# Optimization experiments

Measured on AMD Instinct MI355X. Metric: run time of the kernel, lower is better.

Reference implementation:

```python
import jax, jax.numpy as jnp
import numpy as np

E = 16           # num_experts
D = 4096         # hidden_size
F = 688          # per-expert SwiGLU intermediate size
N = 8192         # total tokens (bsz*seq_len)
CAP_FACTOR = 1.25


def setup_inputs() -> dict:
    key = jax.random.key(0)
    k1, k2, k3, k4, k5, k6 = jax.random.split(key, 6)
    return {
        "x": jax.random.normal(k1, (N, D), dtype=jnp.float32),
        "topk_idx": jax.random.randint(k2, (N,), 0, E, dtype=jnp.int32),
        "topk_scores": jax.random.uniform(k3, (N,), dtype=jnp.float32),
        "Wg": jax.random.normal(k4, (E, D, F), dtype=jnp.float32) * 0.02,
        "Wu": jax.random.normal(k5, (E, D, F), dtype=jnp.float32) * 0.02,
        "Wd": jax.random.normal(k6, (E, F, D), dtype=jnp.float32) * 0.02,
    }


def reference(x, topk_idx, topk_scores, Wg, Wu, Wd):
    # Switch-style top-1 MoE with capacity-based token dropping.
    # Deterministic variant: tokens beyond capacity are dropped in token order
    # (original uses randperm; the math pattern is identical).
    n, d = x.shape
    e = Wg.shape[0]
    cap = int(CAP_FACTOR * n / e)  # static under jit

    # position of each token within its assigned expert (0-based)
    oh = jax.nn.one_hot(topk_idx, e, dtype=jnp.int32)            # [N, E]
    pos = jnp.take_along_axis(jnp.cumsum(oh, axis=0) - 1,
                              topk_idx[:, None].astype(jnp.int32), axis=1)[:, 0]
    keep = pos < cap                                             # [N] bool

    # dispatch: scatter kept tokens into [E, cap, D]; dropped go to dummy row E
    e_safe = jnp.where(keep, topk_idx, e)
    p_safe = jnp.minimum(pos, cap - 1)
    buf = jnp.zeros((e + 1, cap, d), x.dtype).at[e_safe, p_safe].set(x)[:e]

    # per-expert SwiGLU FFN: down(silu(gate(x)) * up(x))
    h = jax.nn.silu(jnp.einsum('ecd,edf->ecf', buf, Wg)) \
        * jnp.einsum('ecd,edf->ecf', buf, Wu)                    # [E, cap, F]
    out = jnp.einsum('ecf,efd->ecd', h, Wd)                      # [E, cap, D]

    # combine: gather back, zero-pad dropped tokens, scale by gate scores
    y = out[topk_idx, p_safe] * keep[:, None].astype(x.dtype)
    y = y * topk_scores[:, None]
    return y
```

## Files before the change

### kernel.cpp

```cpp
#include <hip/hip_runtime.h>
#include <hip/hip_bf16.h>

#define E_ 16
#define D_ 4096
#define F_ 688
#define N_ 8192
#define CAP_ 640
#define NFT_ 11
#define NKT32_ 128
#define NFT32_ 22

typedef __attribute__((ext_vector_type(8))) short bf16x8;
typedef __attribute__((ext_vector_type(4))) float f32x4;
typedef __attribute__((ext_vector_type(4))) float fvec4;
typedef __attribute__((ext_vector_type(4))) unsigned short usvec4;
typedef __attribute__((ext_vector_type(8))) unsigned short usvec8;

__device__ __forceinline__ unsigned short f2bf(float f) {
    __hip_bfloat16 h = __float2bfloat16(f);
    return __builtin_bit_cast(unsigned short, h);
}
__device__ __forceinline__ void gload16(const unsigned short* g, unsigned short* l) {
    __builtin_amdgcn_global_load_lds(
        (const __attribute__((address_space(1))) unsigned int*)g,
        (__attribute__((address_space(3))) unsigned int*)l, 16, 0, 0);
}

#define WAITVN(N) asm volatile("s_waitcnt vmcnt(" #N ")" ::: "memory")
#define SBAR      __builtin_amdgcn_s_barrier()
#define SCHED0    __builtin_amdgcn_sched_barrier(0)


__global__ void k_dispatch(const int* __restrict__ idx,
                           int* __restrict__ slot_token,
                           int* __restrict__ row_of,
                           int* __restrict__ cnt) {
    __shared__ int hist[256][E_];
    const int t = threadIdx.x;
#pragma unroll
    for (int e = 0; e < E_; e++) hist[t][e] = 0;
    __syncthreads();
    const int base = t * (N_ / 256);
    for (int j = 0; j < N_ / 256; j++) {
        int e = idx[base + j];
        hist[t][e]++;
    }
    __syncthreads();
    if (t < E_) {
        int run = 0;
        for (int i = 0; i < 256; i++) { int v = hist[i][t]; hist[i][t] = run; run += v; }
        cnt[t] = run < CAP_ ? run : CAP_;
    }
    for (int s = t; s < E_ * CAP_; s += 256) slot_token[s] = -1;
    __syncthreads();
    for (int j = 0; j < N_ / 256; j++) {
        int i = base + j;
        int e = idx[i];
        int p = hist[t][e]++;
        if (p < CAP_) { slot_token[e * CAP_ + p] = i; row_of[i] = e * CAP_ + p; }
        else          { row_of[i] = -1; }
    }
}

__global__ void k_zero_dropped(const int* __restrict__ row_of, float* __restrict__ y) {
    for (int i = blockIdx.x; i < N_; i += gridDim.x) {
        if (row_of[i] >= 0) continue;
        fvec4* yp = (fvec4*)(y + (size_t)i * D_);
        fvec4 z = {0.f, 0.f, 0.f, 0.f};
        for (int c = threadIdx.x; c < D_ / 4; c += 256) yp[c] = z;
    }
}

__global__ void k_gather(const float* __restrict__ x, const int* __restrict__ slot_token,
                         unsigned short* __restrict__ Aimg) {
    const int strip = blockIdx.y;
    const int kg = blockIdx.x;
    const int t = threadIdx.x;
    const int r = t >> 1, h = t & 1;
    const int tok = slot_token[strip * 128 + r];
#pragma unroll
    for (int i = 0; i < 8; i++) {
        const int kt = kg * 8 + i;
        unsigned short* dst = Aimg + ((size_t)strip * NKT32_ + kt) * 4096;
        usvec8 p0, p1;
        if (tok < 0) {
            usvec8 z = {0, 0, 0, 0, 0, 0, 0, 0};
            p0 = z; p1 = z;
        } else {
            const float* src = x + (size_t)tok * D_ + kt * 32 + h * 16;
            fvec4 a = *(const fvec4*)(src);
            fvec4 b = *(const fvec4*)(src + 4);
            fvec4 c = *(const fvec4*)(src + 8);
            fvec4 d = *(const fvec4*)(src + 12);
            usvec8 q0 = {f2bf(a[0]), f2bf(a[1]), f2bf(a[2]), f2bf(a[3]),
                         f2bf(b[0]), f2bf(b[1]), f2bf(b[2]), f2bf(b[3])};
            usvec8 q1 = {f2bf(c[0]), f2bf(c[1]), f2bf(c[2]), f2bf(c[3]),
                         f2bf(d[0]), f2bf(d[1]), f2bf(d[2]), f2bf(d[3])};
            p0 = q0; p1 = q1;
        }
        *(usvec8*)&dst[(2 * h) * 1024 + r * 8]     = p0;
        *(usvec8*)&dst[(2 * h + 1) * 1024 + r * 8] = p1;
    }
}

__global__ void k_wprep_gu(const float* __restrict__ Wg, const float* __restrict__ Wu,
                           unsigned short* __restrict__ img) {
    const int ft = blockIdx.x, kt = blockIdx.y, e = blockIdx.z;
    const int tid = threadIdx.x;
    const int f4 = (tid & 15) * 4, kq4 = (tid >> 4) * 4;
    const int gf = ft * 64 + f4;
    const bool v = gf < F_;
    const fvec4 fz = {0.f, 0.f, 0.f, 0.f};
    fvec4 g[4], u[4];
#pragma unroll
    for (int r = 0; r < 4; r++) {
        size_t off = (size_t)e * D_ * F_ + (size_t)(kt * 64 + kq4 + r) * F_ + gf;
        g[r] = v ? *(const fvec4*)(Wg + off) : fz;
        u[r] = v ? *(const fvec4*)(Wu + off) : fz;
    }
    const int t32 = kq4 >> 5, kl = kq4 & 31;
    unsigned short* dst = img + ((size_t)(e * NKT32_ + kt * 2 + t32) * NFT_ + ft) * 4096;
    const int ubase = (kl >> 3) * 512 + (kl & 7);
#pragma unroll
    for (int i = 0; i < 4; i++) {
        usvec4 pg = {f2bf(g[0][i]), f2bf(g[1][i]), f2bf(g[2][i]), f2bf(g[3][i])};
        usvec4 pu = {f2bf(u[0][i]), f2bf(u[1][i]), f2bf(u[2][i]), f2bf(u[3][i])};
        *(usvec4*)&dst[ubase + (f4 + i) * 8]        = pg;
        *(usvec4*)&dst[2048 + ubase + (f4 + i) * 8] = pu;
    }
}

__global__ void k_wprep_d(const float* __restrict__ Wd, unsigned short* __restrict__ img) {
    const int dt = blockIdx.x, kt = blockIdx.y, e = blockIdx.z;
    const int tid = threadIdx.x;
    const int d4 = (tid & 15) * 4, kq4 = (tid >> 4) * 4;
    const int gd = dt * 64 + d4;
    const fvec4 fz = {0.f, 0.f, 0.f, 0.f};
    fvec4 b[4];
#pragma unroll
    for (int r = 0; r < 4; r++) {
        int krow = kt * 64 + kq4 + r;
        b[r] = (krow < F_) ? *(const fvec4*)(Wd + (size_t)e * F_ * D_ + (size_t)krow * D_ + gd) : fz;
    }
    const int t32 = kq4 >> 5, kl = kq4 & 31;
    unsigned short* dst = img + ((size_t)(e * NFT32_ + kt * 2 + t32) * 64 + dt) * 2048;
    const int ubase = (kl >> 3) * 512 + (kl & 7);
#pragma unroll
    for (int i = 0; i < 4; i++) {
        usvec4 p = {f2bf(b[0][i]), f2bf(b[1][i]), f2bf(b[2][i]), f2bf(b[3][i])};
        *(usvec4*)&dst[ubase + (d4 + i) * 8] = p;
    }
}

__global__ __launch_bounds__(256, 2) void k_gemm1_dma(
    const unsigned short* __restrict__ Aimg, const unsigned short* __restrict__ Wgu,
    const int* __restrict__ cnt, unsigned short* __restrict__ Himg) {
    const int bid = blockIdx.x;
    const int xcd = bid & 7;
    const int j = bid >> 3;
    const int mb = j % 5;
    const int gl = j / 5;
    const int group = xcd * 22 + gl;
    const int e = group / NFT_, fidx = group % NFT_;
    const int m0 = mb * 128;
    if (m0 >= cnt[e]) return;
    const int strip = e * 5 + mb;

    __shared__ __align__(16) unsigned short Bgu[3][8192];

    const int tid = threadIdx.x;
    const int lane = tid & 63, wave = tid >> 6;
    const int wm = wave & 1, kh = wave >> 1;

    f32x4 accG[4][4], accU[4][4];
#pragma unroll
    for (int a = 0; a < 4; a++)
#pragma unroll
        for (int b = 0; b < 4; b++) {
            f32x4 z = {0.f, 0.f, 0.f, 0.f};
            accG[a][b] = z; accU[a][b] = z;
        }

    const unsigned short* Astrip = Aimg + (size_t)strip * NKT32_ * 4096;
    const unsigned short* WguE = Wgu + ((size_t)e * NKT32_ * NFT_ + fidx) * 4096;
    const int GUS = NFT_ * 4096;
    const int afo = (lane >> 4) * 1024 + (wm * 64 + (lane & 15)) * 8;
    const int bfo = (lane >> 4) * 512 + (lane & 15) * 8;

    bf16x8 a0[4], a1[4];

#define LOADA1(T, S)                                                             \
    {                                                                            \
        const unsigned short* ab = Astrip + (size_t)(2 * (T) + kh) * 4096 + afo; \
        _Pragma("unroll") for (int mf = 0; mf < 4; mf++)                         \
            S[mf] = *(const bf16x8*)(ab + mf * 128);                             \
    }
#define DMAB1(T, BUF)                                                            \
    {                                                                            \
        const unsigned short* bA = WguE + (size_t)(2 * (T)) * GUS;               \
        const unsigned short* bB = bA + GUS;                                     \
        _Pragma("unroll") for (int i = 0; i < 4; i++) {                          \
            const int c = wave * 4 + i;                                          \
            const unsigned short* src = (c < 8) ? (bA + c * 512) : (bB + (c - 8) * 512); \
            gload16(src + lane * 8, &Bgu[BUF][c * 512]);                         \
        }                                                                        \
    }
#define MFMAS1(BUF, S)                                                           \
    {                                                                            \
        __builtin_amdgcn_s_setprio(1);                                           \
        bf16x8 bg[4], bu[4];                                                     \
        _Pragma("unroll") for (int nf = 0; nf < 4; nf++) {                       \
            bg[nf] = *(const bf16x8*)&Bgu[BUF][kh * 4096 + bfo + nf * 128];      \
            bu[nf] = *(const bf16x8*)&Bgu[BUF][kh * 4096 + 2048 + bfo + nf * 128]; \
        }                                                                        \
        _Pragma("unroll") for (int mf = 0; mf < 4; mf++)                         \
        _Pragma("unroll") for (int nf = 0; nf < 4; nf++) {                       \
            accG[mf][nf] = __builtin_amdgcn_mfma_f32_16x16x32_bf16(S[mf], bg[nf], accG[mf][nf], 0, 0, 0); \
            accU[mf][nf] = __builtin_amdgcn_mfma_f32_16x16x32_bf16(S[mf], bu[nf], accU[mf][nf], 0, 0, 0); \
        }                                                                        \
        __builtin_amdgcn_s_setprio(0);                                           \
    }
#define G1IT(T, CS, NS, WN, HA, HB)                                              \
    {                                                                            \
        WAITVN(WN);                                                              \
        SBAR;                                                                    \
        if (HA) { LOADA1((T) + 1, NS) }                                          \
        if (HB) { DMAB1((T) + 2, ((T) + 2) % 3) }                                \
        SCHED0;                                                                  \
        MFMAS1((T) % 3, CS)                                                      \
    }

    LOADA1(0, a0)
    SCHED0;
    DMAB1(0, 0)
    DMAB1(1, 1)
    SCHED0;

    for (int m = 0; m < 31; m++) {
        G1IT(2 * m,     a0, a1, 4, 1, 1)
        G1IT(2 * m + 1, a1, a0, 4, 1, 1)
    }
    G1IT(62, a0, a1, 4, 1, 0)
    G1IT(63, a1, a0, 0, 0, 0)
#undef G1IT
#undef MFMAS1
#undef DMAB1
#undef LOADA1

    {
        float* red = (float*)(&Bgu[0][0]);
#define RED1(ACC)                                                                \
    {                                                                            \
        __syncthreads();                                                         \
        if (kh == 0) {                                                           \
            _Pragma("unroll") for (int mf = 0; mf < 4; mf++)                     \
            _Pragma("unroll") for (int nfl = 0; nfl < 2; nfl++)                  \
                *(f32x4*)&red[(((wm * 2 + 1) * 4 + mf) * 2 + nfl) * 256 + lane * 4] = ACC[mf][2 + nfl]; \
        } else {                                                                 \
            _Pragma("unroll") for (int mf = 0; mf < 4; mf++)                     \
            _Pragma("unroll") for (int nfl = 0; nfl < 2; nfl++)                  \
                *(f32x4*)&red[(((wm * 2 + 0) * 4 + mf) * 2 + nfl) * 256 + lane * 4] = ACC[mf][0 + nfl]; \
        }                                                                        \
        __syncthreads();                                                         \
        if (kh == 0) {                                                           \
            _Pragma("unroll") for (int mf = 0; mf < 4; mf++)                     \
            _Pragma("unroll") for (int nfl = 0; nfl < 2; nfl++) {                \
                f32x4 p = *(const f32x4*)&red[(((wm * 2 + 0) * 4 + mf) * 2 + nfl) * 256 + lane * 4]; \
                ACC[mf][0 + nfl] += p;                                           \
            }                                                                    \
        } else {                                                                 \
            _Pragma("unroll") for (int mf = 0; mf < 4; mf++)                     \
            _Pragma("unroll") for (int nfl = 0; nfl < 2; nfl++) {                \
                f32x4 p = *(const f32x4*)&red[(((wm * 2 + 1) * 4 + mf) * 2 + nfl) * 256 + lane * 4]; \
                ACC[mf][2 + nfl] += p;                                           \
            }                                                                    \
        }                                                                        \
    }
        RED1(accG)
        RED1(accU)
#undef RED1
    }

    unsigned short* Hs = Himg + (size_t)(strip * NFT32_ + fidx * 2) * 4096;
#define EPI1(NB)                                                                 \
    _Pragma("unroll") for (int mf = 0; mf < 4; mf++)                             \
    _Pragma("unroll") for (int nfl = 0; nfl < 2; nfl++) {                        \
        int fl = (NB + nfl) * 16 + (lane & 15);                                  \
        int rl = wm * 64 + mf * 16 + ((lane >> 4) << 2);                         \
        unsigned short* Ht = Hs + (size_t)(fl >> 5) * 4096 + ((fl & 31) >> 3) * 1024 + (fl & 7); \
        _Pragma("unroll") for (int q = 0; q < 4; q++) {                          \
            float g = accG[mf][NB + nfl][q], u = accU[mf][NB + nfl][q];          \
            float h = g * u / (1.f + __expf(-g));                                \
            Ht[(rl + q) * 8] = f2bf(h);                                          \
        }                                                                        \
    }
    if (kh == 0) { EPI1(0) } else { EPI1(2) }
#undef EPI1
}

__global__ __launch_bounds__(256, 3) void k_gemm2_dma(
    const unsigned short* __restrict__ Himg, const unsigned short* __restrict__ WdI,
    const int* __restrict__ slot_token, const int* __restrict__ cnt,
    const float* __restrict__ scores, float* __restrict__ y) {
    const int bid = blockIdx.x;
    const int xcd = bid & 7;
    const int j = bid >> 3;
    const int mb = j % 5;
    const int gl = j / 5;
    const int group = xcd * 128 + gl;
    const int e = group >> 6, didx = group & 63;
    const int m0 = mb * 128, d0 = didx * 64;
    if (m0 >= cnt[e]) return;
    const int strip = e * 5 + mb;

    __shared__ __align__(16) unsigned short Bd[3][4096];
    __shared__ int tokS[128];
    __shared__ float scS[128];

    const int tid = threadIdx.x;
    const int lane = tid & 63, wave = tid >> 6;
    const int wm = wave & 1, kh = wave >> 1;

    if (tid < 128) {
        int t = slot_token[e * CAP_ + m0 + tid];
        tokS[tid] = t;
        scS[tid] = (t >= 0) ? scores[t] : 0.f;
    }
    __syncthreads();

    f32x4 acc[4][4];
#pragma unroll
    for (int a = 0; a < 4; a++)
#pragma unroll
        for (int b = 0; b < 4; b++) {
            f32x4 z = {0.f, 0.f, 0.f, 0.f};
            acc[a][b] = z;
        }

    const unsigned short* Hstrip = Himg + (size_t)strip * NFT32_ * 4096;
    const unsigned short* WdE = WdI + ((size_t)e * NFT32_ * 64 + didx) * 2048;
    const int WDS = 64 * 2048;
    const int afo = (lane >> 4) * 1024 + (wm * 64 + (lane & 15)) * 8;
    const int bfo = (lane >> 4) * 512 + (lane & 15) * 8;

    bf16x8 a0[4], a1[4];

#define LOADA2(T, S)                                                             \
    {                                                                            \
        const unsigned short* ab = Hstrip + (size_t)(2 * (T) + kh) * 4096 + afo; \
        _Pragma("unroll") for (int mf = 0; mf < 4; mf++)                         \
            S[mf] = *(const bf16x8*)(ab + mf * 128);                             \
    }
#define DMAB2(T, BUF)                                                            \
    {                                                                            \
        const unsigned short* bA = WdE + (size_t)(2 * (T)) * WDS;                \
        const unsigned short* bB = bA + WDS;                                     \
        _Pragma("unroll") for (int i = 0; i < 2; i++) {                          \
            const int c = wave * 2 + i;                                          \
            const unsigned short* src = (c < 4) ? (bA + c * 512) : (bB + (c - 4) * 512); \
            gload16(src + lane * 8, &Bd[BUF][c * 512]);                          \
        }                                                                        \
    }
#define MFMAS2(BUF, S)                                                           \
    {                                                                            \
        __builtin_amdgcn_s_setprio(1);                                           \
        bf16x8 bv[4];                                                            \
        _Pragma("unroll") for (int nf = 0; nf < 4; nf++)                         \
            bv[nf] = *(const bf16x8*)&Bd[BUF][kh * 2048 + bfo + nf * 128];       \
        _Pragma("unroll") for (int mf = 0; mf < 4; mf++)                         \
        _Pragma("unroll") for (int nf = 0; nf < 4; nf++)                         \
            acc[mf][nf] = __builtin_amdgcn_mfma_f32_16x16x32_bf16(S[mf], bv[nf], acc[mf][nf], 0, 0, 0); \
        __builtin_amdgcn_s_setprio(0);                                           \
    }
#define G2IT(T, CS, NS, WN, HA, HB)                                              \
    {                                                                            \
        WAITVN(WN);                                                              \
        SBAR;                                                                    \
        if (HA) { LOADA2((T) + 1, NS) }                                          \
        if (HB) { DMAB2((T) + 2, ((T) + 2) % 3) }                                \
        SCHED0;                                                                  \
        MFMAS2((T) % 3, CS)                                                      \
    }

    LOADA2(0, a0)
    SCHED0;
    DMAB2(0, 0)
    DMAB2(1, 1)
    SCHED0;

    G2IT(0, a0, a1, 2, 1, 1)
    G2IT(1, a1, a0, 2, 1, 1)
    G2IT(2, a0, a1, 2, 1, 1)
    G2IT(3, a1, a0, 2, 1, 1)
    G2IT(4, a0, a1, 2, 1, 1)
    G2IT(5, a1, a0, 2, 1, 1)
    G2IT(6, a0, a1, 2, 1, 1)
    G2IT(7, a1, a0, 2, 1, 1)
    G2IT(8, a0, a1, 2, 1, 1)
    G2IT(9, a1, a0, 2, 1, 0)
    G2IT(10, a0, a1, 0, 0, 0)
#undef G2IT
#undef MFMAS2
#undef DMAB2
#undef LOADA2

    {
        float* red = (float*)(&Bd[0][0]);
#define RED2(MH)                                                                 \
    {                                                                            \
        __syncthreads();                                                         \
        if (kh == 0) {                                                           \
            _Pragma("unroll") for (int mfl = 0; mfl < 2; mfl++)                  \
            _Pragma("unroll") for (int nfl = 0; nfl < 2; nfl++)                  \
                *(f32x4*)&red[((((wm * 2 + 1) * 2 + mfl) * 2 + nfl)) * 256 + lane * 4] = acc[(MH) * 2 + mfl][2 + nfl]; \
        } else {                                                                 \
            _Pragma("unroll") for (int mfl = 0; mfl < 2; mfl++)                  \
            _Pragma("unroll") for (int nfl = 0; nfl < 2; nfl++)                  \
                *(f32x4*)&red[((((wm * 2 + 0) * 2 + mfl) * 2 + nfl)) * 256 + lane * 4] = acc[(MH) * 2 + mfl][0 + nfl]; \
        }                                                                        \
        __syncthreads();                                                         \
        if (kh == 0) {                                                           \
            _Pragma("unroll") for (int mfl = 0; mfl < 2; mfl++)                  \
            _Pragma("unroll") for (int nfl = 0; nfl < 2; nfl++) {                \
                f32x4 p = *(const f32x4*)&red[((((wm * 2 + 0) * 2 + mfl) * 2 + nfl)) * 256 + lane * 4]; \
                acc[(MH) * 2 + mfl][0 + nfl] += p;                               \
            }                                                                    \
        } else {                                                                 \
            _Pragma("unroll") for (int mfl = 0; mfl < 2; mfl++)                  \
            _Pragma("unroll") for (int nfl = 0; nfl < 2; nfl++) {                \
                f32x4 p = *(const f32x4*)&red[((((wm * 2 + 1) * 2 + mfl) * 2 + nfl)) * 256 + lane * 4]; \
                acc[(MH) * 2 + mfl][2 + nfl] += p;                               \
            }                                                                    \
        }                                                                        \
    }
        RED2(0)
        RED2(1)
#undef RED2
    }

#define EPI2(NB)                                                                 \
    _Pragma("unroll") for (int mf = 0; mf < 4; mf++)                             \
    _Pragma("unroll") for (int nfl = 0; nfl < 2; nfl++) {                        \
        int d = d0 + (NB + nfl) * 16 + (lane & 15);                              \
        int rowb = wm * 64 + mf * 16 + ((lane >> 4) << 2);                       \
        _Pragma("unroll") for (int q = 0; q < 4; q++) {                          \
            int row = rowb + q;                                                  \
            int t = tokS[row];                                                   \
            if (t >= 0) y[(size_t)t * D_ + d] = acc[mf][NB + nfl][q] * scS[row]; \
        }                                                                        \
    }
    if (kh == 0) { EPI2(0) } else { EPI2(2) }
#undef EPI2
}

extern "C" void kernel_launch(void* const* d_in, const int* in_sizes, int n_in,
                              void* d_out, int out_size, void* d_ws, size_t ws_size,
                              hipStream_t stream) {
    const float* x   = (const float*)d_in[0];
    const int*   idx = (const int*)d_in[1];
    const float* sc  = (const float*)d_in[2];
    const float* Wg  = (const float*)d_in[3];
    const float* Wu  = (const float*)d_in[4];
    const float* Wd  = (const float*)d_in[5];
    float* y = (float*)d_out;

    char* ws = (char*)d_ws;
    int* slot_token = (int*)ws;
    int* row_of     = (int*)(ws + 40960);
    int* cnt        = (int*)(ws + 40960 + 32768);
    const size_t hoff   = 131072;
    const size_t hbytes = (size_t)80 * NFT32_ * 8192;
    unsigned short* Himg = (unsigned short*)(ws + hoff);
    const size_t aoff   = hoff + hbytes;
    const size_t abytes = (size_t)80 * NKT32_ * 8192;
    unsigned short* Aimg = (unsigned short*)(ws + aoff);
    const size_t guoff   = aoff + abytes;
    const size_t gubytes = (size_t)E_ * NKT32_ * NFT_ * 8192;
    unsigned short* WguI = (unsigned short*)(ws + guoff);
    const size_t wdoff   = guoff + gubytes;
    unsigned short* WdI  = (unsigned short*)(ws + wdoff);

    k_dispatch<<<1, 256, 0, stream>>>(idx, slot_token, row_of, cnt);
    k_zero_dropped<<<128, 256, 0, stream>>>(row_of, y);
    k_gather<<<dim3(16, 80), 256, 0, stream>>>(x, slot_token, Aimg);
    k_wprep_gu<<<dim3(NFT_, 64, E_), 256, 0, stream>>>(Wg, Wu, WguI);
    k_wprep_d<<<dim3(64, NFT_, E_), 256, 0, stream>>>(Wd, WdI);
    k_gemm1_dma<<<880, 256, 0, stream>>>(Aimg, WguI, cnt, Himg);
    k_gemm2_dma<<<5120, 256, 0, stream>>>(Himg, WdI, slot_token, cnt, sc, y);
}
```

Baseline: 510.1 us.

## Widen weight-prep stores to 16-byte chunks and raise GEMM occupancy bounds

The weight conversion kernels now have each thread convert 8 consecutive k-rows of one matrix and write full 16-byte bf16 vectors, instead of 4 rows with 8-byte stores for both gate and up. The gate/up prep splits the block's threads between Wg and Wu, and the down-projection prep covers two d-tiles per block, so it launches half as many blocks. This targets fragmented partial stores in the fp32-to-bf16 prep, which reads and writes several hundred MB per call. Separately, the launch bounds of both GEMM kernels go up by one block per SM. That may force register spills if the compiler cannot fit the new limit.

```diff
diff --git a/kernel.cpp b/kernel.cpp
--- a/kernel.cpp
+++ b/kernel.cpp
@@ -107,52 +107,58 @@
                            unsigned short* __restrict__ img) {
     const int ft = blockIdx.x, kt = blockIdx.y, e = blockIdx.z;
     const int tid = threadIdx.x;
-    const int f4 = (tid & 15) * 4, kq4 = (tid >> 4) * 4;
+    const int mat = tid >> 7;
+    const int f4 = (tid & 15) * 4;
+    const int kq8 = ((tid >> 4) & 7) * 8;
     const int gf = ft * 64 + f4;
     const bool v = gf < F_;
+    const float* W = mat ? Wu : Wg;
     const fvec4 fz = {0.f, 0.f, 0.f, 0.f};
-    fvec4 g[4], u[4];
-#pragma unroll
-    for (int r = 0; r < 4; r++) {
-        size_t off = (size_t)e * D_ * F_ + (size_t)(kt * 64 + kq4 + r) * F_ + gf;
-        g[r] = v ? *(const fvec4*)(Wg + off) : fz;
-        u[r] = v ? *(const fvec4*)(Wu + off) : fz;
-    }
-    const int t32 = kq4 >> 5, kl = kq4 & 31;
-    unsigned short* dst = img + ((size_t)(e * NKT32_ + kt * 2 + t32) * NFT_ + ft) * 4096;
-    const int ubase = (kl >> 3) * 512 + (kl & 7);
+    fvec4 w[8];
+#pragma unroll
+    for (int r = 0; r < 8; r++) {
+        size_t off = (size_t)e * D_ * F_ + (size_t)(kt * 64 + kq8 + r) * F_ + gf;
+        w[r] = v ? *(const fvec4*)(W + off) : fz;
+    }
+    const int t32 = kq8 >> 5;
+    const int kgp = (kq8 & 31) >> 3;
+    unsigned short* dst = img + ((size_t)(e * NKT32_ + kt * 2 + t32) * NFT_ + ft) * 4096
+                              + mat * 2048 + kgp * 512;
 #pragma unroll
     for (int i = 0; i < 4; i++) {
-        usvec4 pg = {f2bf(g[0][i]), f2bf(g[1][i]), f2bf(g[2][i]), f2bf(g[3][i])};
-        usvec4 pu = {f2bf(u[0][i]), f2bf(u[1][i]), f2bf(u[2][i]), f2bf(u[3][i])};
-        *(usvec4*)&dst[ubase + (f4 + i) * 8]        = pg;
-        *(usvec4*)&dst[2048 + ubase + (f4 + i) * 8] = pu;
+        usvec8 p = {f2bf(w[0][i]), f2bf(w[1][i]), f2bf(w[2][i]), f2bf(w[3][i]),
+                    f2bf(w[4][i]), f2bf(w[5][i]), f2bf(w[6][i]), f2bf(w[7][i])};
+        *(usvec8*)&dst[(f4 + i) * 8] = p;
     }
 }
 
 __global__ void k_wprep_d(const float* __restrict__ Wd, unsigned short* __restrict__ img) {
-    const int dt = blockIdx.x, kt = blockIdx.y, e = blockIdx.z;
+    const int kt = blockIdx.y, e = blockIdx.z;
     const int tid = threadIdx.x;
-    const int d4 = (tid & 15) * 4, kq4 = (tid >> 4) * 4;
+    const int dt = blockIdx.x * 2 + (tid >> 7);
+    const int d4 = (tid & 15) * 4;
+    const int kq8 = ((tid >> 4) & 7) * 8;
     const int gd = dt * 64 + d4;
     const fvec4 fz = {0.f, 0.f, 0.f, 0.f};
-    fvec4 b[4];
-#pragma unroll
-    for (int r = 0; r < 4; r++) {
-        int krow = kt * 64 + kq4 + r;
+    fvec4 b[8];
+#pragma unroll
+    for (int r = 0; r < 8; r++) {
+        int krow = kt * 64 + kq8 + r;
         b[r] = (krow < F_) ? *(const fvec4*)(Wd + (size_t)e * F_ * D_ + (size_t)krow * D_ + gd) : fz;
     }
-    const int t32 = kq4 >> 5, kl = kq4 & 31;
-    unsigned short* dst = img + ((size_t)(e * NFT32_ + kt * 2 + t32) * 64 + dt) * 2048;
-    const int ubase = (kl >> 3) * 512 + (kl & 7);
+    const int t32 = kq8 >> 5;
+    const int kgp = (kq8 & 31) >> 3;
+    unsigned short* dst = img + ((size_t)(e * NFT32_ + kt * 2 + t32) * 64 + dt) * 2048
+                              + kgp * 512;
 #pragma unroll
     for (int i = 0; i < 4; i++) {
-        usvec4 p = {f2bf(b[0][i]), f2bf(b[1][i]), f2bf(b[2][i]), f2bf(b[3][i])};
-        *(usvec4*)&dst[ubase + (d4 + i) * 8] = p;
-    }
-}
-
-__global__ __launch_bounds__(256, 2) void k_gemm1_dma(
+        usvec8 p = {f2bf(b[0][i]), f2bf(b[1][i]), f2bf(b[2][i]), f2bf(b[3][i]),
+                    f2bf(b[4][i]), f2bf(b[5][i]), f2bf(b[6][i]), f2bf(b[7][i])};
+        *(usvec8*)&dst[(d4 + i) * 8] = p;
+    }
+}
+
+__global__ __launch_bounds__(256, 3) void k_gemm1_dma(
     const unsigned short* __restrict__ Aimg, const unsigned short* __restrict__ Wgu,
     const int* __restrict__ cnt, unsigned short* __restrict__ Himg) {
     const int bid = blockIdx.x;
@@ -298,7 +304,7 @@
 #undef EPI1
 }
 
-__global__ __launch_bounds__(256, 3) void k_gemm2_dma(
+__global__ __launch_bounds__(256, 4) void k_gemm2_dma(
     const unsigned short* __restrict__ Himg, const unsigned short* __restrict__ WdI,
     const int* __restrict__ slot_token, const int* __restrict__ cnt,
     const float* __restrict__ scores, float* __restrict__ y) {
@@ -484,7 +490,7 @@
     k_zero_dropped<<<128, 256, 0, stream>>>(row_of, y);
     k_gather<<<dim3(16, 80), 256, 0, stream>>>(x, slot_token, Aimg);
     k_wprep_gu<<<dim3(NFT_, 64, E_), 256, 0, stream>>>(Wg, Wu, WguI);
-    k_wprep_d<<<dim3(64, NFT_, E_), 256, 0, stream>>>(Wd, WdI);
+    k_wprep_d<<<dim3(32, NFT_, E_), 256, 0, stream>>>(Wd, WdI);
     k_gemm1_dma<<<880, 256, 0, stream>>>(Aimg, WguI, cnt, Himg);
     k_gemm2_dma<<<5120, 256, 0, stream>>>(Himg, WdI, slot_token, cnt, sc, y);
 }
```

New measurement: 1.294 ms. 2.54x slower.
